# Optimization experiments

Measured on AMD Instinct MI355X. Metric: run time of the kernel, lower is better.

The kernel has to match this reference:

```python
import jax, jax.numpy as jnp
import numpy as np

B, DIM1, DIM2, DIM3 = 4, 2048, 4096, 4096


def setup_inputs() -> dict:
    key = jax.random.key(0)
    k1, k2, k3 = jax.random.split(key, 3)
    x = jax.random.normal(k1, (B, DIM1, DIM2), dtype=jnp.float32)
    y = jax.random.normal(k2, (B, DIM1, DIM3), dtype=jnp.float32)
    weight = jax.random.normal(k3, (DIM2, DIM3), dtype=jnp.float32)
    return {"x": x, "y": y, "weight": weight}


def reference(x, y, weight):
    # Out = hardswish(mish(leaky_relu(x @ W, 0.01) + y)) + 0.5
    v = jnp.einsum('bik,kn->bin', x, weight)              # (B, dim1, dim3)
    v = jnp.where(v >= 0, v, 0.01 * v)                    # LeakyReLU(0.01)
    v = v + y
    v = v * jnp.tanh(jax.nn.softplus(v))                  # Mish
    relu6 = jnp.clip(v + 3.0, 0.0, 6.0)
    v = v * relu6 * (1.0 / 6.0) + 0.5                     # HardSwish + 0.5 (baked into kernel)
    return v
```

## Files before the change

### kernel.cpp

```cpp
#include <hip/hip_runtime.h>
#include <hip/hip_bf16.h>
#include <cstdint>

typedef __attribute__((ext_vector_type(8))) short short8;
typedef __attribute__((ext_vector_type(4))) float f32x4;
typedef __attribute__((ext_vector_type(16))) float f32x16;
typedef unsigned short ushort_t;

#define MM 8192
#define NN 4096
#define KK 4096

#define BM 128
#define BN 128
#define BK 64
#define NT (KK / BK)

#define MFMA_BF16 __builtin_amdgcn_mfma_f32_16x16x32_bf16
#define MFMA32 __builtin_amdgcn_mfma_f32_32x32x16_bf16

__device__ __forceinline__ ushort_t f2bf(float f) {
  uint32_t u = __builtin_bit_cast(uint32_t, f);
  u = (u + 0x7FFFu + ((u >> 16) & 1u)) >> 16;
  return (ushort_t)u;
}

__device__ __forceinline__ float epilogue(float v, float yv) {
  v = fmaxf(v, 0.01f * v);
  v += yv;
  const float vc = fminf(v, 15.f);
  const float t = __builtin_amdgcn_exp2f(vc * 1.44269504f);
  const float d = t * t + 2.f * t;
  const float mi = v * d * __builtin_amdgcn_rcpf(d + 2.f);
  const float r6 = fminf(fmaxf(mi + 3.f, 0.f), 6.f);
  return mi * r6 * (1.f / 6.f) + 0.5f;
}

__device__ __forceinline__ void gload_lds16(const void* g, void* l) {
  __builtin_amdgcn_global_load_lds(
      (const __attribute__((address_space(1))) unsigned int*)g,
      (__attribute__((address_space(3))) unsigned int*)l, 16, 0, 0);
}

#define CVT_BLOCKS ((MM * KK) / (256 * 8))
#define WT_BLOCKS ((NN / 32) * (KK / 32))

template <int DO_X>
__global__ void prep_kernel(const float* __restrict__ X, ushort_t* __restrict__ XB,
                            const float* __restrict__ W, ushort_t* __restrict__ WT) {
  __shared__ float t[32][33];
  const int bid = blockIdx.x;
  const int tid = threadIdx.x;
  if (DO_X && bid < CVT_BLOCKS) {
    const size_t i = ((size_t)bid * 256 + tid) * 8;
    f32x4 v0 = __builtin_nontemporal_load(reinterpret_cast<const f32x4*>(&X[i]));
    f32x4 v1 = __builtin_nontemporal_load(reinterpret_cast<const f32x4*>(&X[i + 4]));
    short8 o;
    o[0] = (short)f2bf(v0[0]); o[1] = (short)f2bf(v0[1]);
    o[2] = (short)f2bf(v0[2]); o[3] = (short)f2bf(v0[3]);
    o[4] = (short)f2bf(v1[0]); o[5] = (short)f2bf(v1[1]);
    o[6] = (short)f2bf(v1[2]); o[7] = (short)f2bf(v1[3]);
    *reinterpret_cast<short8*>(&XB[i]) = o;
  } else {
    const int b2 = DO_X ? (bid - CVT_BLOCKS) : bid;
    const int n0 = (b2 & 127) * 32, k0 = (b2 >> 7) * 32;
    const int tx = tid & 31, ty = tid >> 5;
#pragma unroll
    for (int i = ty; i < 32; i += 8)
      t[i][tx] = __builtin_nontemporal_load(&W[(size_t)(k0 + i) * NN + n0 + tx]);
    __syncthreads();
#pragma unroll
    for (int i = ty; i < 32; i += 8)
      WT[(size_t)(n0 + i) * KK + k0 + tx] = f2bf(t[tx][i]);
  }
}

#define HB 32768

#define STAGE(base, kt)                                                        \
  _Pragma("unroll") for (int c = 0; c < 4; ++c) {                              \
    gload_lds16(XB + offA[c] + (kt), (base) + (wid * 8 + c * 64) * 64);        \
    gload_lds16(WT + offB[c] + (kt),                                           \
                (base) + 16384 + (wid * 8 + c * 64) * 64);                     \
  }

__global__ __launch_bounds__(512, 2) void gemm_bf16_v5(
    const ushort_t* __restrict__ XB, const ushort_t* __restrict__ WT,
    const float* __restrict__ Y, float* __restrict__ O) {
  __shared__ ushort_t sh[2 * HB];

  const int wg = blockIdx.x;
  const int xcd = wg & 7;
  const int local = wg >> 3;
  const int bm0 = (local >> 1) * 256;
  const int bn0 = (xcd * 2 + (local & 1)) * 256;

  const int tid = threadIdx.x;
  const int lane = tid & 63;
  const int wid = tid >> 6;
  const int wmi = wid >> 2;
  const int wni = wid & 3;

  const int l8 = lane >> 3;
  const uint32_t vsw = (uint32_t)l8 * KK + ((lane & 7) ^ l8) * 8;
  uint32_t offA[4], offB[4];
#pragma unroll
  for (int c = 0; c < 4; ++c) {
    offA[c] = (uint32_t)(bm0 + wid * 8 + c * 64) * KK + vsw;
    offB[c] = (uint32_t)(bn0 + wid * 8 + c * 64) * KK + vsw;
  }

  const int l31 = lane & 31, kh = lane >> 5, l7 = lane & 7;
  const int aBase = (wmi * 128 + l31) * 64;
  const int bBase = 16384 + (wni * 64 + l31) * 64;
  int sl[4];
#pragma unroll
  for (int ks = 0; ks < 4; ++ks) sl[ks] = ((ks * 2 + kh) ^ l7) * 8;

  f32x16 acc[4][2] = {};

  STAGE(sh, 0);
  __syncthreads();

#pragma unroll 1
  for (int t = 0; t < NT; ++t) {
    ushort_t* cur = sh + (t & 1) * HB;
    ushort_t* nxt = sh + ((t + 1) & 1) * HB;
    const int k1 = ((t + 1) & (NT - 1)) * BK;
    STAGE(nxt, k1);
#pragma unroll
    for (int ks = 0; ks < 4; ++ks) {
      short8 av[4], bv[2];
#pragma unroll
      for (int mf = 0; mf < 4; ++mf)
        av[mf] = *reinterpret_cast<const short8*>(&cur[aBase + mf * 2048 + sl[ks]]);
#pragma unroll
      for (int nf = 0; nf < 2; ++nf)
        bv[nf] = *reinterpret_cast<const short8*>(&cur[bBase + nf * 2048 + sl[ks]]);
#pragma unroll
      for (int mf = 0; mf < 4; ++mf)
#pragma unroll
        for (int nf = 0; nf < 2; ++nf)
          acc[mf][nf] = MFMA32(av[mf], bv[nf], acc[mf][nf], 0, 0, 0);
    }
    __syncthreads();
  }

#pragma unroll
  for (int mf = 0; mf < 4; ++mf) {
#pragma unroll
    for (int nf = 0; nf < 2; ++nf) {
#pragma unroll
      for (int r = 0; r < 16; ++r) {
        const int grow = bm0 + wmi * 128 + mf * 32 + (r & 3) + 8 * (r >> 2) + 4 * kh;
        const int gcol = bn0 + wni * 64 + nf * 32 + l31;
        const size_t idx = (size_t)grow * NN + gcol;
        const float yv = __builtin_nontemporal_load(&Y[idx]);
        __builtin_nontemporal_store(epilogue(acc[mf][nf][r], yv), &O[idx]);
      }
    }
  }
}

#define LDP 72
__global__ __launch_bounds__(256, 3) void gemm_fused(
    const float* __restrict__ X, const ushort_t* __restrict__ WT,
    const float* __restrict__ Y, float* __restrict__ O) {
  __shared__ ushort_t Asm[BM * LDP];
  __shared__ ushort_t Bsm[BN * LDP];

  const int nwg = (MM / BM) * (NN / BN);
  int wg = blockIdx.x;
  wg = (wg % 8) * (nwg / 8) + wg / 8;
  const int NTC = NN / BN;
  const int bm0 = (wg / NTC) * BM;
  const int bn0 = (wg % NTC) * BN;

  const int tid = threadIdx.x;
  const int lane = tid & 63;
  const int wid = tid >> 6;
  const int wm = (wid >> 1) * 64, wn = (wid & 1) * 64;
  const int lr = lane & 15, lg = lane >> 4;

  f32x4 acc[4][4] = {};

  const int arow = tid >> 2;
  const int ac = (tid & 3) * 4;
  const int brow = tid >> 1;
  const int bc0 = (tid & 1) * 32;

  for (int kt = 0; kt < KK; kt += BK) {
    __syncthreads();
#pragma unroll
    for (int p = 0; p < 2; ++p) {
      const int row = arow + p * 64;
      const float* src = &X[(size_t)(bm0 + row) * KK + kt];
#pragma unroll
      for (int j = 0; j < 4; ++j) {
        f32x4 v = *reinterpret_cast<const f32x4*>(&src[ac + j * 16]);
        uint2 packed;
        packed.x = (uint32_t)f2bf(v[0]) | ((uint32_t)f2bf(v[1]) << 16);
        packed.y = (uint32_t)f2bf(v[2]) | ((uint32_t)f2bf(v[3]) << 16);
        *reinterpret_cast<uint2*>(&Asm[row * LDP + ac + j * 16]) = packed;
      }
    }
    {
      const ushort_t* src = &WT[(size_t)(bn0 + brow) * KK + kt + bc0];
#pragma unroll
      for (int j = 0; j < 4; ++j) {
        short8 u = *reinterpret_cast<const short8*>(&src[j * 8]);
        *reinterpret_cast<short8*>(&Bsm[brow * LDP + bc0 + j * 8]) = u;
      }
    }
    __syncthreads();

#pragma unroll
    for (int ks = 0; ks < 2; ++ks) {
      short8 a[4], b[4];
#pragma unroll
      for (int i = 0; i < 4; ++i) {
        a[i] = *reinterpret_cast<const short8*>(&Asm[(wm + i * 16 + lr) * LDP + ks * 32 + lg * 8]);
        b[i] = *reinterpret_cast<const short8*>(&Bsm[(wn + i * 16 + lr) * LDP + ks * 32 + lg * 8]);
      }
#pragma unroll
      for (int i = 0; i < 4; ++i)
#pragma unroll
        for (int j = 0; j < 4; ++j)
          acc[i][j] = MFMA_BF16(a[i], b[j], acc[i][j], 0, 0, 0);
    }
  }

#pragma unroll
  for (int i = 0; i < 4; ++i) {
#pragma unroll
    for (int j = 0; j < 4; ++j) {
#pragma unroll
      for (int r = 0; r < 4; ++r) {
        const int grow = bm0 + wm + i * 16 + lg * 4 + r;
        const int gcol = bn0 + wn + j * 16 + lr;
        const size_t idx = (size_t)grow * NN + gcol;
        O[idx] = epilogue(acc[i][j][r], Y[idx]);
      }
    }
  }
}

__global__ void naive_fused(const float* __restrict__ X, const float* __restrict__ W,
                            const float* __restrict__ Y, float* __restrict__ O) {
  const int n0 = (blockIdx.x * 256 + threadIdx.x) * 4;
  const int m = blockIdx.y;
  f32x4 acc = {0.f, 0.f, 0.f, 0.f};
  const float* xr = &X[(size_t)m * KK];
  for (int k = 0; k < KK; ++k) {
    const float xv = xr[k];
    const f32x4 wv = *reinterpret_cast<const f32x4*>(&W[(size_t)k * NN + n0]);
    acc[0] += xv * wv[0];
    acc[1] += xv * wv[1];
    acc[2] += xv * wv[2];
    acc[3] += xv * wv[3];
  }
  const size_t idx = (size_t)m * NN + n0;
  O[idx + 0] = epilogue(acc[0], Y[idx + 0]);
  O[idx + 1] = epilogue(acc[1], Y[idx + 1]);
  O[idx + 2] = epilogue(acc[2], Y[idx + 2]);
  O[idx + 3] = epilogue(acc[3], Y[idx + 3]);
}

extern "C" void kernel_launch(void* const* d_in, const int* in_sizes, int n_in,
                              void* d_out, int out_size, void* d_ws, size_t ws_size,
                              hipStream_t stream) {
  const float* x = (const float*)d_in[0];
  const float* y = (const float*)d_in[1];
  const float* w = (const float*)d_in[2];
  float* out = (float*)d_out;

  const size_t xb_bytes = (size_t)MM * KK * sizeof(ushort_t);
  const size_t wt_bytes = (size_t)NN * KK * sizeof(ushort_t);

  if (ws_size >= xb_bytes + wt_bytes) {
    ushort_t* XB = (ushort_t*)d_ws;
    ushort_t* WT = (ushort_t*)((char*)d_ws + xb_bytes);
    hipLaunchKernelGGL((prep_kernel<1>), dim3(CVT_BLOCKS + WT_BLOCKS), dim3(256), 0, stream,
                       x, XB, w, WT);
    hipLaunchKernelGGL(gemm_bf16_v5, dim3((MM / 256) * (NN / 256)), dim3(512), 0, stream,
                       XB, WT, y, out);
  } else if (ws_size >= wt_bytes) {
    ushort_t* WT = (ushort_t*)d_ws;
    hipLaunchKernelGGL((prep_kernel<0>), dim3(WT_BLOCKS), dim3(256), 0, stream,
                       x, nullptr, w, WT);
    hipLaunchKernelGGL(gemm_fused, dim3((MM / BM) * (NN / BN)), dim3(256), 0, stream,
                       x, WT, y, out);
  } else {
    hipLaunchKernelGGL(naive_fused, dim3(NN / 1024, MM), dim3(256), 0, stream, x, w, y, out);
  }
}
```

Before: 332.1 us.

## Load B operand directly from global into registers with one-tile prefetch

The weight operand is no longer staged through LDS. Each wave reads its B fragments straight from global memory into registers, one k-tile ahead, interleaved with the MFMA groups. Only A stays in the double-buffered LDS, which halves shared memory per block, and s_setprio is raised around the MFMA bursts. This aims to cut LDS traffic and the staging cost for B, at the price of more VGPRs, B reads duplicated across the two M-waves, and narrower, less coalesced global loads whose latency now has to be hidden within a single tile.

```diff
diff --git a/kernel.cpp b/kernel.cpp
--- a/kernel.cpp
+++ b/kernel.cpp
@@ -75,16 +75,37 @@
   }
 }
 
-#define HB 32768
-
-#define STAGE(base, kt)                                                        \
-  _Pragma("unroll") for (int c = 0; c < 4; ++c) {                              \
-    gload_lds16(XB + offA[c] + (kt), (base) + (wid * 8 + c * 64) * 64);        \
-    gload_lds16(WT + offB[c] + (kt),                                           \
-                (base) + 16384 + (wid * 8 + c * 64) * 64);                     \
-  }
-
-__global__ __launch_bounds__(512, 2) void gemm_bf16_v5(
+#define HB 16384
+
+#define STAGE_A4(base, kv)                                                     \
+  _Pragma("unroll") for (int c = 0; c < 4; ++c)                                \
+      gload_lds16(XB + offA[c] + (kv), (base) + (wid * 8 + c * 64) * 64);
+
+#define LDC(off) (*reinterpret_cast<const short8*>(&cur[off]))
+
+#define RDA(ks)                                                                \
+  av0 = LDC(aBase + 0 * 2048 + sl##ks);                                        \
+  av1 = LDC(aBase + 1 * 2048 + sl##ks);                                        \
+  av2 = LDC(aBase + 2 * 2048 + sl##ks);                                        \
+  av3 = LDC(aBase + 3 * 2048 + sl##ks);
+
+#define LDB(d0, d1, kv, ksc)                                                   \
+  d0 = *reinterpret_cast<const short8*>(WT + uB0 + (kv) + (ksc)*16);           \
+  d1 = *reinterpret_cast<const short8*>(WT + uB1 + (kv) + (ksc)*16);
+
+#define MFB(B0, B1)                                                            \
+  __builtin_amdgcn_s_setprio(1);                                               \
+  acc[0][0] = MFMA32(av0, B0, acc[0][0], 0, 0, 0);                             \
+  acc[0][1] = MFMA32(av0, B1, acc[0][1], 0, 0, 0);                             \
+  acc[1][0] = MFMA32(av1, B0, acc[1][0], 0, 0, 0);                             \
+  acc[1][1] = MFMA32(av1, B1, acc[1][1], 0, 0, 0);                             \
+  acc[2][0] = MFMA32(av2, B0, acc[2][0], 0, 0, 0);                             \
+  acc[2][1] = MFMA32(av2, B1, acc[2][1], 0, 0, 0);                             \
+  acc[3][0] = MFMA32(av3, B0, acc[3][0], 0, 0, 0);                             \
+  acc[3][1] = MFMA32(av3, B1, acc[3][1], 0, 0, 0);                             \
+  __builtin_amdgcn_s_setprio(0);
+
+__global__ __launch_bounds__(512, 2) void gemm_bf16_v8(
     const ushort_t* __restrict__ XB, const ushort_t* __restrict__ WT,
     const float* __restrict__ Y, float* __restrict__ O) {
   __shared__ ushort_t sh[2 * HB];
@@ -103,46 +124,50 @@
 
   const int l8 = lane >> 3;
   const uint32_t vsw = (uint32_t)l8 * KK + ((lane & 7) ^ l8) * 8;
-  uint32_t offA[4], offB[4];
-#pragma unroll
-  for (int c = 0; c < 4; ++c) {
+  uint32_t offA[4];
+#pragma unroll
+  for (int c = 0; c < 4; ++c)
     offA[c] = (uint32_t)(bm0 + wid * 8 + c * 64) * KK + vsw;
-    offB[c] = (uint32_t)(bn0 + wid * 8 + c * 64) * KK + vsw;
-  }
 
   const int l31 = lane & 31, kh = lane >> 5, l7 = lane & 7;
   const int aBase = (wmi * 128 + l31) * 64;
-  const int bBase = 16384 + (wni * 64 + l31) * 64;
-  int sl[4];
-#pragma unroll
-  for (int ks = 0; ks < 4; ++ks) sl[ks] = ((ks * 2 + kh) ^ l7) * 8;
+  const int sl0 = ((0 + kh) ^ l7) * 8;
+  const int sl1 = ((2 + kh) ^ l7) * 8;
+  const int sl2 = ((4 + kh) ^ l7) * 8;
+  const int sl3 = ((6 + kh) ^ l7) * 8;
+
+  const uint32_t uB0 = (uint32_t)(bn0 + wni * 64 + 0 * 32 + l31) * KK + kh * 8;
+  const uint32_t uB1 = (uint32_t)(bn0 + wni * 64 + 1 * 32 + l31) * KK + kh * 8;
 
   f32x16 acc[4][2] = {};
-
-  STAGE(sh, 0);
+  short8 av0, av1, av2, av3;
+  short8 bA0, bA1, bB0, bB1, bC0, bC1, bD0, bD1;
+
+  STAGE_A4(sh, 0);
+  LDB(bA0, bA1, 0, 0);
+  LDB(bB0, bB1, 0, 1);
+  LDB(bC0, bC1, 0, 2);
+  LDB(bD0, bD1, 0, 3);
   __syncthreads();
 
 #pragma unroll 1
   for (int t = 0; t < NT; ++t) {
-    ushort_t* cur = sh + (t & 1) * HB;
+    const ushort_t* cur = sh + (t & 1) * HB;
     ushort_t* nxt = sh + ((t + 1) & 1) * HB;
     const int k1 = ((t + 1) & (NT - 1)) * BK;
-    STAGE(nxt, k1);
-#pragma unroll
-    for (int ks = 0; ks < 4; ++ks) {
-      short8 av[4], bv[2];
-#pragma unroll
-      for (int mf = 0; mf < 4; ++mf)
-        av[mf] = *reinterpret_cast<const short8*>(&cur[aBase + mf * 2048 + sl[ks]]);
-#pragma unroll
-      for (int nf = 0; nf < 2; ++nf)
-        bv[nf] = *reinterpret_cast<const short8*>(&cur[bBase + nf * 2048 + sl[ks]]);
-#pragma unroll
-      for (int mf = 0; mf < 4; ++mf)
-#pragma unroll
-        for (int nf = 0; nf < 2; ++nf)
-          acc[mf][nf] = MFMA32(av[mf], bv[nf], acc[mf][nf], 0, 0, 0);
-    }
+    STAGE_A4(nxt, k1);
+    RDA(0);
+    MFB(bA0, bA1);
+    LDB(bA0, bA1, k1, 0);
+    RDA(1);
+    MFB(bB0, bB1);
+    LDB(bB0, bB1, k1, 1);
+    RDA(2);
+    MFB(bC0, bC1);
+    LDB(bC0, bC1, k1, 2);
+    RDA(3);
+    MFB(bD0, bD1);
+    LDB(bD0, bD1, k1, 3);
     __syncthreads();
   }
 
@@ -282,7 +307,7 @@
     ushort_t* WT = (ushort_t*)((char*)d_ws + xb_bytes);
     hipLaunchKernelGGL((prep_kernel<1>), dim3(CVT_BLOCKS + WT_BLOCKS), dim3(256), 0, stream,
                        x, XB, w, WT);
-    hipLaunchKernelGGL(gemm_bf16_v5, dim3((MM / 256) * (NN / 256)), dim3(512), 0, stream,
+    hipLaunchKernelGGL(gemm_bf16_v8, dim3((MM / 256) * (NN / 256)), dim3(512), 0, stream,
                        XB, WT, y, out);
   } else if (ws_size >= wt_bytes) {
     ushort_t* WT = (ushort_t*)d_ws;
```

Measured after the change: 434.7 us. 1.31x slower.

## Replace 256x256 double-buffered GEMM with 128x128 single-buffer tiles

Applied to the files above, without the earlier changes.

Swaps the 512-thread, 256x256-tile, double-buffered LDS GEMM for a 256-thread kernel with 128x128 tiles, one LDS buffer and two barriers per K step. Each wave now holds a 2x2 set of 32x32 MFMA accumulators instead of 4x2. The aim is higher occupancy (4 blocks per CU) to hide latency in place of explicit prefetch. In exchange it loses load/compute overlap within a block and halves operand reuse per LDS and global load, which raises memory traffic.

```diff
diff --git a/kernel.cpp b/kernel.cpp
--- a/kernel.cpp
+++ b/kernel.cpp
@@ -75,85 +75,75 @@
   }
 }
 
-#define HB 32768
-
-#define STAGE(base, kt)                                                        \
-  _Pragma("unroll") for (int c = 0; c < 4; ++c) {                              \
-    gload_lds16(XB + offA[c] + (kt), (base) + (wid * 8 + c * 64) * 64);        \
-    gload_lds16(WT + offB[c] + (kt),                                           \
-                (base) + 16384 + (wid * 8 + c * 64) * 64);                     \
-  }
-
-__global__ __launch_bounds__(512, 2) void gemm_bf16_v5(
+__global__ __launch_bounds__(256, 4) void gemm_bf16_r10(
     const ushort_t* __restrict__ XB, const ushort_t* __restrict__ WT,
     const float* __restrict__ Y, float* __restrict__ O) {
-  __shared__ ushort_t sh[2 * HB];
+  __shared__ ushort_t As[BM * BK];
+  __shared__ ushort_t Bs[BN * BK];
 
   const int wg = blockIdx.x;
   const int xcd = wg & 7;
   const int local = wg >> 3;
-  const int bm0 = (local >> 1) * 256;
-  const int bn0 = (xcd * 2 + (local & 1)) * 256;
+  const int bm0 = (local >> 2) * BM;
+  const int bn0 = (xcd * 4 + (local & 3)) * BN;
 
   const int tid = threadIdx.x;
   const int lane = tid & 63;
   const int wid = tid >> 6;
-  const int wmi = wid >> 2;
-  const int wni = wid & 3;
-
-  const int l8 = lane >> 3;
-  const uint32_t vsw = (uint32_t)l8 * KK + ((lane & 7) ^ l8) * 8;
+  const int wm = (wid >> 1) * 64, wn = (wid & 1) * 64;
+
+  const int s_sub = lane >> 3;
+  const int s_chunk = (lane & 7) ^ s_sub;
   uint32_t offA[4], offB[4];
 #pragma unroll
-  for (int c = 0; c < 4; ++c) {
-    offA[c] = (uint32_t)(bm0 + wid * 8 + c * 64) * KK + vsw;
-    offB[c] = (uint32_t)(bn0 + wid * 8 + c * 64) * KK + vsw;
+  for (int j = 0; j < 4; ++j) {
+    const int srow = wid * 32 + j * 8 + s_sub;
+    offA[j] = (uint32_t)(bm0 + srow) * KK + s_chunk * 8;
+    offB[j] = (uint32_t)(bn0 + srow) * KK + s_chunk * 8;
   }
 
   const int l31 = lane & 31, kh = lane >> 5, l7 = lane & 7;
-  const int aBase = (wmi * 128 + l31) * 64;
-  const int bBase = 16384 + (wni * 64 + l31) * 64;
-  int sl[4];
-#pragma unroll
-  for (int ks = 0; ks < 4; ++ks) sl[ks] = ((ks * 2 + kh) ^ l7) * 8;
-
-  f32x16 acc[4][2] = {};
-
-  STAGE(sh, 0);
-  __syncthreads();
+  const int aBase = (wm + l31) * BK;
+  const int bBase = (wn + l31) * BK;
+  const int sl0 = ((0 + kh) ^ l7) * 8;
+  const int sl1 = ((2 + kh) ^ l7) * 8;
+  const int sl2 = ((4 + kh) ^ l7) * 8;
+  const int sl3 = ((6 + kh) ^ l7) * 8;
+
+  f32x16 acc[2][2] = {};
 
 #pragma unroll 1
-  for (int t = 0; t < NT; ++t) {
-    ushort_t* cur = sh + (t & 1) * HB;
-    ushort_t* nxt = sh + ((t + 1) & 1) * HB;
-    const int k1 = ((t + 1) & (NT - 1)) * BK;
-    STAGE(nxt, k1);
+  for (int kt = 0; kt < KK; kt += BK) {
+    __syncthreads();
+#pragma unroll
+    for (int j = 0; j < 4; ++j) {
+      gload_lds16(XB + offA[j] + kt, As + (wid * 4 + j) * 512);
+      gload_lds16(WT + offB[j] + kt, Bs + (wid * 4 + j) * 512);
+    }
+    __syncthreads();
+
 #pragma unroll
     for (int ks = 0; ks < 4; ++ks) {
-      short8 av[4], bv[2];
-#pragma unroll
-      for (int mf = 0; mf < 4; ++mf)
-        av[mf] = *reinterpret_cast<const short8*>(&cur[aBase + mf * 2048 + sl[ks]]);
-#pragma unroll
-      for (int nf = 0; nf < 2; ++nf)
-        bv[nf] = *reinterpret_cast<const short8*>(&cur[bBase + nf * 2048 + sl[ks]]);
-#pragma unroll
-      for (int mf = 0; mf < 4; ++mf)
-#pragma unroll
-        for (int nf = 0; nf < 2; ++nf)
-          acc[mf][nf] = MFMA32(av[mf], bv[nf], acc[mf][nf], 0, 0, 0);
-    }
-    __syncthreads();
-  }
-
-#pragma unroll
-  for (int mf = 0; mf < 4; ++mf) {
+      const int sl = (ks == 0) ? sl0 : (ks == 1) ? sl1 : (ks == 2) ? sl2 : sl3;
+      short8 a0 = *reinterpret_cast<const short8*>(&As[aBase + 0 * 2048 + sl]);
+      short8 a1 = *reinterpret_cast<const short8*>(&As[aBase + 1 * 2048 + sl]);
+      short8 b0 = *reinterpret_cast<const short8*>(&Bs[bBase + 0 * 2048 + sl]);
+      short8 b1 = *reinterpret_cast<const short8*>(&Bs[bBase + 1 * 2048 + sl]);
+      acc[0][0] = MFMA32(a0, b0, acc[0][0], 0, 0, 0);
+      acc[0][1] = MFMA32(a0, b1, acc[0][1], 0, 0, 0);
+      acc[1][0] = MFMA32(a1, b0, acc[1][0], 0, 0, 0);
+      acc[1][1] = MFMA32(a1, b1, acc[1][1], 0, 0, 0);
+    }
+  }
+
+#pragma unroll
+  for (int mf = 0; mf < 2; ++mf) {
 #pragma unroll
     for (int nf = 0; nf < 2; ++nf) {
 #pragma unroll
       for (int r = 0; r < 16; ++r) {
-        const int grow = bm0 + wmi * 128 + mf * 32 + (r & 3) + 8 * (r >> 2) + 4 * kh;
-        const int gcol = bn0 + wni * 64 + nf * 32 + l31;
+        const int grow = bm0 + wm + mf * 32 + (r & 3) + 8 * (r >> 2) + 4 * kh;
+        const int gcol = bn0 + wn + nf * 32 + l31;
         const size_t idx = (size_t)grow * NN + gcol;
         const float yv = __builtin_nontemporal_load(&Y[idx]);
         __builtin_nontemporal_store(epilogue(acc[mf][nf][r], yv), &O[idx]);
@@ -282,7 +272,7 @@
     ushort_t* WT = (ushort_t*)((char*)d_ws + xb_bytes);
     hipLaunchKernelGGL((prep_kernel<1>), dim3(CVT_BLOCKS + WT_BLOCKS), dim3(256), 0, stream,
                        x, XB, w, WT);
-    hipLaunchKernelGGL(gemm_bf16_v5, dim3((MM / 256) * (NN / 256)), dim3(512), 0, stream,
+    hipLaunchKernelGGL(gemm_bf16_r10, dim3((MM / BM) * (NN / BN)), dim3(256), 0, stream,
                        XB, WT, y, out);
   } else if (ws_size >= wt_bytes) {
     ushort_t* WT = (ushort_t*)d_ws;
```

Result: slower. 374.8 us (+12.8%).
